# Kernel optimization log

Hardware: AMD Instinct MI355X
Metric: run time of the kernel (lower is better)

The kernel has to match this reference:

```python
import jax, jax.numpy as jnp
import numpy as np

N_NODES = 50000
N_EDGES = 800000
D = 64
VOCAB = 1000
NUM_ITERS = 2
BN_EPS = 1e-5


def _bn(h, g, b):
    # BatchNorm1d in training mode: batch statistics over the edge dim, biased var
    mu = h.mean(axis=0)
    var = h.var(axis=0)
    return g * (h - mu) * jax.lax.rsqrt(var + BN_EPS) + b


def _edge_agg(x, idx_i, idx_j, W1, b1, g1, be1, W2, b2, g2, be2):
    # gather -> concat -> Linear+BN+ReLU x2 -> scatter-sum to idx_i -> degree norm
    m = jnp.concatenate([x[idx_i], x[idx_j]], axis=1)          # [E, 2D]
    h = jax.nn.relu(_bn(m @ W1 + b1, g1, be1))                  # [E, D]
    h = jax.nn.relu(_bn(h @ W2 + b2, g2, be2))                  # [E, D]
    agg = jax.ops.segment_sum(h, idx_i, num_segments=N_NODES)   # [N, D]
    deg = jax.ops.segment_sum(jnp.ones((idx_i.shape[0],), x.dtype), idx_i,
                              num_segments=N_NODES)
    deg_inv = jnp.where(deg > 0, 1.0 / deg, 0.0)
    return deg_inv[:, None] * agg


def setup_inputs() -> dict:
    key = jax.random.key(0)
    ks = jax.random.split(key, 24)
    s = 0.05
    inp = {
        'nodes': jax.random.randint(ks[0], (N_NODES,), 0, VOCAB),
        'edges': jax.random.randint(ks[1], (2, N_EDGES), 0, N_NODES),
        'emb': jax.random.normal(ks[2], (VOCAB, D), jnp.float32) * s,
        # parent aggregation MLP
        'p_W1': jax.random.normal(ks[3], (2 * D, D), jnp.float32) * s,
        'p_b1': jnp.zeros((D,), jnp.float32),
        'p_g1': jnp.ones((D,), jnp.float32),
        'p_be1': jnp.zeros((D,), jnp.float32),
        'p_W2': jax.random.normal(ks[4], (D, D), jnp.float32) * s,
        'p_b2': jnp.zeros((D,), jnp.float32),
        'p_g2': jnp.ones((D,), jnp.float32),
        'p_be2': jnp.zeros((D,), jnp.float32),
        # child aggregation MLP
        'c_W1': jax.random.normal(ks[5], (2 * D, D), jnp.float32) * s,
        'c_b1': jnp.zeros((D,), jnp.float32),
        'c_g1': jnp.ones((D,), jnp.float32),
        'c_be1': jnp.zeros((D,), jnp.float32),
        'c_W2': jax.random.normal(ks[6], (D, D), jnp.float32) * s,
        'c_b2': jnp.zeros((D,), jnp.float32),
        'c_g2': jnp.ones((D,), jnp.float32),
        'c_be2': jnp.zeros((D,), jnp.float32),
        # final aggregation (dropout = identity, eval semantics)
        'fc_W': jax.random.normal(ks[7], (3 * D, 2 * D), jnp.float32) * s,
        'fc_b': jnp.zeros((2 * D,), jnp.float32),
        'fc2_W': jax.random.normal(ks[8], (2 * D, D), jnp.float32) * s,
        'fc2_b': jnp.zeros((D,), jnp.float32),
        # Conv1d(D, 2D, kernel=1) == Linear D -> 2D
        'conv_W': jax.random.normal(ks[9], (D, 2 * D), jnp.float32) * s,
        'conv_b': jnp.zeros((2 * D,), jnp.float32),
    }
    return inp


def reference(nodes, edges, emb, p_W1, p_b1, p_g1, p_be1, p_W2, p_b2, p_g2, p_be2,
              c_W1, c_b1, c_g1, c_be1, c_W2, c_b2, c_g2, c_be2,
              fc_W, fc_b, fc2_W, fc2_b, conv_W, conv_b):
    src, dst = edges[0], edges[1]
    x = emb[nodes]                                            # [N, D]
    for _ in range(NUM_ITERS):
        # ParentAggregation: flow source_to_target -> x_i = x[dst], x_j = x[src], scatter to dst
        fi = _edge_agg(x, dst, src, p_W1, p_b1, p_g1, p_be1, p_W2, p_b2, p_g2, p_be2)
        # ChildAggregation: flow target_to_source -> x_i = x[src], x_j = x[dst], scatter to src
        fo = _edge_agg(x, src, dst, c_W1, c_b1, c_g1, c_be1, c_W2, c_b2, c_g2, c_be2)
        cat = jnp.concatenate([x, fi, fo], axis=1)            # [N, 3D]
        upd = jax.nn.relu(cat @ fc_W + fc_b) @ fc2_W + fc2_b  # [N, D]
        x = x + upd
    return x @ conv_W + conv_b                                # [N, 2D]
```

## Files before the change

### kernel.cpp

```cpp
#include <hip/hip_runtime.h>

#define NN 50000
#define NE 800000
#define BN_EPS 1e-5f
#define SCAN_T 256
#define SCAN_NB ((NN + SCAN_T - 1) / SCAN_T)

#define BKT_SH 8
#define NBKT ((NN + 255) >> 8)
#define CAP 6144
#define PCH 4096
#define NPB ((NE + PCH - 1) / PCH)

#define ST_SUM1 0
#define ST_SQ1 64
#define ST_CROSS 128
#define ST_SUM2 192
#define ST_SSQ2 256
#define ST_AGG 320

using bf16x8 = __attribute__((ext_vector_type(8))) __bf16;
using bf16x4 = __attribute__((ext_vector_type(4))) __bf16;
using floatx4 = __attribute__((ext_vector_type(4))) float;

#define MFMA16(a, b, c) __builtin_amdgcn_mfma_f32_16x16x32_bf16(a, b, c, 0, 0, 0)

__device__ __forceinline__ bf16x8 load_wfrag(const float* W, int ncols, int kb, int ct, int lane) {
  int col = ct * 16 + (lane & 15);
  int k0 = kb * 32 + ((lane >> 4) << 3);
  bf16x8 f;
#pragma unroll
  for (int j = 0; j < 8; ++j) f[j] = (__bf16)W[(k0 + j) * ncols + col];
  return f;
}

__global__ void k_setup(const int* __restrict__ nodes, const float* __restrict__ emb,
                        float* __restrict__ x, int* __restrict__ bcur) {
  int tid = blockIdx.x * blockDim.x + threadIdx.x;
  int stride = gridDim.x * blockDim.x;
  for (int idx = tid; idx < NN * 64; idx += stride)
    x[idx] = emb[nodes[idx >> 6] * 64 + (idx & 63)];
  for (int t = tid; t < 2 * NBKT; t += stride)
    bcur[t] = (t < NBKT ? t : t - NBKT) * CAP;
}

__global__ void __launch_bounds__(256) k_part(const int* __restrict__ src,
                                              const int* __restrict__ dst,
                                              int* __restrict__ bcur,
                                              unsigned int* __restrict__ stage) {
  const int dir = blockIdx.y;
  const int* key = dir ? src : dst;
  int* bc = bcur + dir * NBKT;
  unsigned int* st = stage + (size_t)dir * NBKT * CAP;
  __shared__ int lh[256];
  __shared__ int sb[256];
  __shared__ int lbase[NBKT];
  __shared__ unsigned int pay[PCH];
  const int tid = threadIdx.x;
  lh[tid] = 0;
  __syncthreads();
  const int c0 = blockIdx.x * PCH;
  const int nv = (NE - c0 < PCH) ? (NE - c0) : PCH;
  unsigned int rk[PCH / 256];
#pragma unroll
  for (int i = 0; i < PCH / 256; ++i) {
    int l = i * 256 + tid;
    if (l < nv) {
      int b = key[c0 + l] >> BKT_SH;
      int r = atomicAdd(&lh[b], 1);
      rk[i] = ((unsigned)b << 13) | (unsigned)r;
    } else {
      rk[i] = 0xFFFFFFFFu;
    }
  }
  __syncthreads();
  int cntv = lh[tid];
  sb[tid] = cntv;
  __syncthreads();
  for (int o = 1; o < 256; o <<= 1) {
    int u = (tid >= o) ? sb[tid - o] : 0;
    __syncthreads();
    sb[tid] += u;
    __syncthreads();
  }
  int excl = sb[tid] - cntv;
  __syncthreads();
  sb[tid] = excl;
  if (tid < NBKT && cntv > 0) lbase[tid] = atomicAdd(&bc[tid], cntv);
  __syncthreads();
#pragma unroll
  for (int i = 0; i < PCH / 256; ++i) {
    if (rk[i] != 0xFFFFFFFFu) {
      int e = c0 + i * 256 + tid;
      int b = (int)(rk[i] >> 13);
      int r = (int)(rk[i] & 0x1FFFu);
      unsigned int s = (unsigned)src[e], d = (unsigned)dst[e];
      pay[sb[b] + r] = dir ? ((s << 16) | d) : ((d << 16) | s);
    }
  }
  __syncthreads();
  for (int t = tid; t < nv; t += 256) {
    int lo = 0, hi = 255;
    while (lo < hi) {
      int mid = (lo + hi + 1) >> 1;
      if (sb[mid] <= t) lo = mid; else hi = mid - 1;
    }
    st[lbase[lo] + (t - sb[lo])] = pay[t];
  }
}

__global__ void __launch_bounds__(256) k_count(const int* __restrict__ bcur,
                                               const unsigned int* __restrict__ stage,
                                               int* __restrict__ cnt_d, int* __restrict__ cnt_s) {
  const int dir = blockIdx.y;
  const int b = blockIdx.x;
  int* cnt = dir ? cnt_s : cnt_d;
  const unsigned int* st = stage + (size_t)dir * NBKT * CAP + (size_t)b * CAP;
  __shared__ int lc[256];
  lc[threadIdx.x] = 0;
  __syncthreads();
  int sz = bcur[dir * NBKT + b] - b * CAP;
  for (int t = threadIdx.x; t < sz; t += 256)
    atomicAdd(&lc[(st[t] >> 16) - (b << BKT_SH)], 1);
  __syncthreads();
  int n = (b << BKT_SH) + threadIdx.x;
  if (n < NN) cnt[n] = lc[threadIdx.x];
}

__global__ void k_scan1(const int* __restrict__ cnt_d, const int* __restrict__ cnt_s,
                        int* __restrict__ off_d, int* __restrict__ off_s, int* __restrict__ btot) {
  const int* cnt = blockIdx.y ? cnt_s : cnt_d;
  int* off = blockIdx.y ? off_s : off_d;
  __shared__ int sm[SCAN_T];
  int i = blockIdx.x * SCAN_T + threadIdx.x;
  int v = (i < NN) ? cnt[i] : 0;
  sm[threadIdx.x] = v;
  __syncthreads();
  for (int o = 1; o < SCAN_T; o <<= 1) {
    int u = (threadIdx.x >= o) ? sm[threadIdx.x - o] : 0;
    __syncthreads();
    sm[threadIdx.x] += u;
    __syncthreads();
  }
  if (i < NN) off[i] = sm[threadIdx.x];
  if (threadIdx.x == SCAN_T - 1) btot[blockIdx.y * SCAN_NB + blockIdx.x] = sm[SCAN_T - 1];
}

__global__ void k_scan2(int* __restrict__ btot) {
  __shared__ int sm[SCAN_T];
  int t = threadIdx.x;
  for (int y = 0; y < 2; ++y) {
    int v = (t < SCAN_NB) ? btot[y * SCAN_NB + t] : 0;
    sm[t] = v;
    __syncthreads();
    for (int o = 1; o < SCAN_T; o <<= 1) {
      int u = (t >= o) ? sm[t - o] : 0;
      __syncthreads();
      sm[t] += u;
      __syncthreads();
    }
    if (t < SCAN_NB) btot[y * SCAN_NB + t] = sm[t] - v;
    __syncthreads();
  }
}

__global__ void k_scan3(const int* __restrict__ cnt_d, const int* __restrict__ cnt_s,
                        int* __restrict__ off_d, int* __restrict__ off_s,
                        const int* __restrict__ btot, float* __restrict__ dinv_d,
                        float* __restrict__ dinv_s) {
  const int* cnt = blockIdx.y ? cnt_s : cnt_d;
  int* off = blockIdx.y ? off_s : off_d;
  float* dinv = blockIdx.y ? dinv_s : dinv_d;
  int i = blockIdx.x * SCAN_T + threadIdx.x;
  if (i < NN) {
    int incl = off[i];
    int c = cnt[i];
    int o = incl - c + btot[blockIdx.y * SCAN_NB + blockIdx.x];
    off[i] = o;
    dinv[i] = c > 0 ? 1.0f / (float)c : 0.f;
  }
  if (i == NN - 1) off[NN] = NE;
}

__global__ void __launch_bounds__(256) k_fill2(const int* __restrict__ bcur,
                                               const unsigned int* __restrict__ stage,
                                               const int* __restrict__ off_d,
                                               const int* __restrict__ off_s,
                                               unsigned short* __restrict__ jl_d,
                                               unsigned short* __restrict__ jl_s,
                                               unsigned short* __restrict__ il_d,
                                               unsigned short* __restrict__ il_s) {
  const int dir = blockIdx.y;
  const int b = blockIdx.x;
  const int* off = dir ? off_s : off_d;
  unsigned short* jl = dir ? jl_s : jl_d;
  unsigned short* il = dir ? il_s : il_d;
  const unsigned int* st = stage + (size_t)dir * NBKT * CAP + (size_t)b * CAP;
  __shared__ int lcur[256];
  __shared__ unsigned short ljl[CAP];
  __shared__ unsigned short lil[CAP];
  int csr0 = off[b << BKT_SH];
  int n = (b << BKT_SH) + threadIdx.x;
  lcur[threadIdx.x] = (n < NN) ? off[n] - csr0 : 0;
  __syncthreads();
  int sz = bcur[dir * NBKT + b] - b * CAP;
  for (int t = threadIdx.x; t < sz; t += 256) {
    unsigned int v = st[t];
    int p = atomicAdd(&lcur[(v >> 16) - (b << BKT_SH)], 1);
    ljl[p] = (unsigned short)(v & 0xFFFFu);
    lil[p] = (unsigned short)(v >> 16);
  }
  __syncthreads();
  for (int t = threadIdx.x; t < sz; t += 256) {
    jl[csr0 + t] = ljl[t];
    il[csr0 + t] = lil[t];
  }
}

__global__ void __launch_bounds__(256) k_node_xform(
    const float* __restrict__ x, const float* __restrict__ W1,
    __bf16* __restrict__ Ab, __bf16* __restrict__ Bb,
    float* __restrict__ stats, int do_zero) {
  const int lane = threadIdx.x & 63;
  const int wid = threadIdx.x >> 6;
  __shared__ alignas(16) __bf16 xb[4][16 * 72];
  if (do_zero && blockIdx.x == 0)
    for (int t = threadIdx.x; t < 2 * ST_AGG; t += blockDim.x) stats[t] = 0.f;
  bf16x8 wfa[4][2], wfb[4][2];
#pragma unroll
  for (int ct = 0; ct < 4; ++ct)
#pragma unroll
    for (int kb = 0; kb < 2; ++kb) {
      wfa[ct][kb] = load_wfrag(W1, 64, kb, ct, lane);
      wfb[ct][kb] = load_wfrag(W1 + 64 * 64, 64, kb, ct, lane);
    }
  __bf16* vb = xb[wid];
  int wgid = (blockIdx.x * blockDim.x + threadIdx.x) >> 6;
  int nw = (gridDim.x * blockDim.x) >> 6;
  for (int tile = wgid; tile < NN / 16; tile += nw) {
#pragma unroll
    for (int t = 0; t < 16; ++t)
      vb[t * 72 + lane] = (__bf16)x[(tile * 16 + t) * 64 + lane];
    const bf16x8 a0 = *(const bf16x8*)&vb[(lane & 15) * 72 + ((lane >> 4) << 3)];
    const bf16x8 a1 = *(const bf16x8*)&vb[(lane & 15) * 72 + 32 + ((lane >> 4) << 3)];
#pragma unroll
    for (int ct = 0; ct < 4; ++ct) {
      floatx4 aA = {0.f, 0.f, 0.f, 0.f}, aB = {0.f, 0.f, 0.f, 0.f};
      aA = MFMA16(a0, wfa[ct][0], aA);
      aA = MFMA16(a1, wfa[ct][1], aA);
      aB = MFMA16(a0, wfb[ct][0], aB);
      aB = MFMA16(a1, wfb[ct][1], aB);
#pragma unroll
      for (int r = 0; r < 4; ++r) {
        int row = ((lane >> 4) << 2) + r;
        int o = (tile * 16 + row) * 64 + ct * 16 + (lane & 15);
        Ab[o] = (__bf16)aA[r];
        Bb[o] = (__bf16)aB[r];
      }
    }
  }
}

__global__ void __launch_bounds__(256) k_node_stats(
    const __bf16* __restrict__ Ap, const __bf16* __restrict__ Bp,
    const __bf16* __restrict__ Ac, const __bf16* __restrict__ Bc,
    const int* __restrict__ cnt_d, const int* __restrict__ cnt_s,
    float* __restrict__ stats) {
  const int lane = threadIdx.x & 63;
  const int g = lane >> 4, q = lane & 15;
  __shared__ float sacc[256];
  for (int t = threadIdx.x; t < 256; t += blockDim.x) sacc[t] = 0.f;
  __syncthreads();
  float sp[4] = {0, 0, 0, 0}, qp[4] = {0, 0, 0, 0};
  float sc[4] = {0, 0, 0, 0}, qc[4] = {0, 0, 0, 0};
  int wgid = (blockIdx.x * blockDim.x + threadIdx.x) >> 6;
  int nw = (gridDim.x * blockDim.x) >> 6;
  for (int ch = wgid; ch < NN / 4; ch += nw) {
    int n = ch * 4 + g;
    float wd = (float)cnt_d[n];
    float ws = (float)cnt_s[n];
    bf16x4 ap = *(const bf16x4*)(Ap + n * 64 + 4 * q);
    bf16x4 bp = *(const bf16x4*)(Bp + n * 64 + 4 * q);
    bf16x4 ac = *(const bf16x4*)(Ac + n * 64 + 4 * q);
    bf16x4 bc = *(const bf16x4*)(Bc + n * 64 + 4 * q);
#pragma unroll
    for (int k = 0; k < 4; ++k) {
      float a = (float)ap[k], b = (float)bp[k], c = (float)ac[k], d = (float)bc[k];
      sp[k] += wd * a + ws * b;
      qp[k] += wd * a * a + ws * b * b;
      sc[k] += ws * c + wd * d;
      qc[k] += ws * c * c + wd * d * d;
    }
  }
#pragma unroll
  for (int k = 0; k < 4; ++k) {
    sp[k] += __shfl_xor(sp[k], 16); sp[k] += __shfl_xor(sp[k], 32);
    qp[k] += __shfl_xor(qp[k], 16); qp[k] += __shfl_xor(qp[k], 32);
    sc[k] += __shfl_xor(sc[k], 16); sc[k] += __shfl_xor(sc[k], 32);
    qc[k] += __shfl_xor(qc[k], 16); qc[k] += __shfl_xor(qc[k], 32);
  }
  if (lane < 16) {
#pragma unroll
    for (int k = 0; k < 4; ++k) {
      atomicAdd(&sacc[4 * q + k], sp[k]);
      atomicAdd(&sacc[64 + 4 * q + k], qp[k]);
      atomicAdd(&sacc[128 + 4 * q + k], sc[k]);
      atomicAdd(&sacc[192 + 4 * q + k], qc[k]);
    }
  }
  __syncthreads();
  for (int t = threadIdx.x; t < 256; t += blockDim.x) {
    int dstoff = (t < 128) ? t : ST_AGG + (t - 128);
    atomicAdd(&stats[dstoff], sacc[t]);
  }
}

__global__ void __launch_bounds__(256) k_cross_csr2(
    const unsigned short* __restrict__ il, const unsigned short* __restrict__ jl,
    const __bf16* __restrict__ Ap, const __bf16* __restrict__ Bp,
    const __bf16* __restrict__ Ac, const __bf16* __restrict__ Bc,
    float* __restrict__ stats) {
  const int lane = threadIdx.x & 63;
  const int c8 = lane & 7, e8 = lane >> 3;
  __shared__ float sacc[128];
  for (int t = threadIdx.x; t < 128; t += blockDim.x) sacc[t] = 0.f;
  __syncthreads();
  float cp[8] = {0, 0, 0, 0, 0, 0, 0, 0}, cc[8] = {0, 0, 0, 0, 0, 0, 0, 0};
  int wgid = (blockIdx.x * blockDim.x + threadIdx.x) >> 6;
  int nw = (gridDim.x * blockDim.x) >> 6;
  for (int tile = wgid; tile < NE / 16; tile += nw) {
    int e0 = tile * 16;
    int iv = (int)il[e0 + (lane & 15)];
    int jv = (int)jl[e0 + (lane & 15)];
#pragma unroll
    for (int r = 0; r < 2; ++r) {
      int ee = r * 8 + e8;
      int i = __shfl(iv, ee);
      int j = __shfl(jv, ee);
      bf16x8 ap = *(const bf16x8*)(Ap + (size_t)i * 64 + c8 * 8);
      bf16x8 bp = *(const bf16x8*)(Bp + (size_t)j * 64 + c8 * 8);
      bf16x8 ac = *(const bf16x8*)(Ac + (size_t)j * 64 + c8 * 8);
      bf16x8 bc = *(const bf16x8*)(Bc + (size_t)i * 64 + c8 * 8);
#pragma unroll
      for (int k = 0; k < 8; ++k) {
        cp[k] += (float)ap[k] * (float)bp[k];
        cc[k] += (float)ac[k] * (float)bc[k];
      }
    }
  }
#pragma unroll
  for (int k = 0; k < 8; ++k) {
    cp[k] += __shfl_xor(cp[k], 8);  cp[k] += __shfl_xor(cp[k], 16); cp[k] += __shfl_xor(cp[k], 32);
    cc[k] += __shfl_xor(cc[k], 8);  cc[k] += __shfl_xor(cc[k], 16); cc[k] += __shfl_xor(cc[k], 32);
  }
  if (lane < 8) {
#pragma unroll
    for (int k = 0; k < 8; ++k) {
      atomicAdd(&sacc[lane * 8 + k], cp[k]);
      atomicAdd(&sacc[64 + lane * 8 + k], cc[k]);
    }
  }
  __syncthreads();
  for (int t = threadIdx.x; t < 128; t += blockDim.x) {
    int dstoff = (t < 64) ? (ST_CROSS + t) : (ST_AGG + ST_CROSS + (t - 64));
    atomicAdd(&stats[dstoff], sacc[t]);
  }
}

__global__ void __launch_bounds__(256) k_edge_stats_csr2(
    const unsigned short* __restrict__ il, const unsigned short* __restrict__ jl,
    const __bf16* __restrict__ Ap, const __bf16* __restrict__ Bp,
    const __bf16* __restrict__ Ac, const __bf16* __restrict__ Bc,
    const float* __restrict__ pg1, const float* __restrict__ pbe1,
    const float* __restrict__ cg1, const float* __restrict__ cbe1,
    const float* __restrict__ pW2, const float* __restrict__ cW2,
    float* __restrict__ stats) {
  const int lane = threadIdx.x & 63;
  const int wid = threadIdx.x >> 6;
  const int g = lane >> 4, q = lane & 15;
  const int c8 = lane & 7;
  const int e8 = lane >> 3;
  __shared__ alignas(16) __bf16 vbuf[4][2][16 * 72];
  __shared__ float sred[256];
  float s1p[8], t1p[8], s1c[8], t1c[8];
#pragma unroll
  for (int k = 0; k < 8; ++k) {
    int c = c8 * 8 + k;
    float mu = stats[ST_SUM1 + c] * (1.f / NE);
    float var = (stats[ST_SQ1 + c] + 2.f * stats[ST_CROSS + c]) * (1.f / NE) - mu * mu;
    float s = pg1[c] * rsqrtf(var + BN_EPS);
    s1p[k] = s;
    t1p[k] = pbe1[c] - mu * s;
    mu = stats[ST_AGG + ST_SUM1 + c] * (1.f / NE);
    var = (stats[ST_AGG + ST_SQ1 + c] + 2.f * stats[ST_AGG + ST_CROSS + c]) * (1.f / NE) - mu * mu;
    s = cg1[c] * rsqrtf(var + BN_EPS);
    s1c[k] = s;
    t1c[k] = cbe1[c] - mu * s;
  }
  bf16x8 wfp[4][2], wfc[4][2];
#pragma unroll
  for (int ct = 0; ct < 4; ++ct)
#pragma unroll
    for (int kb = 0; kb < 2; ++kb) {
      wfp[ct][kb] = load_wfrag(pW2, 64, kb, ct, lane);
      wfc[ct][kb] = load_wfrag(cW2, 64, kb, ct, lane);
    }
  float sump[4] = {0, 0, 0, 0}, ssqp[4] = {0, 0, 0, 0};
  float sumc[4] = {0, 0, 0, 0}, ssqc[4] = {0, 0, 0, 0};
  __bf16* vbp = vbuf[wid][0];
  __bf16* vbc = vbuf[wid][1];
  int wgid = (blockIdx.x * blockDim.x + threadIdx.x) >> 6;
  int nw = (gridDim.x * blockDim.x) >> 6;
  for (int tile = wgid; tile < NE / 16; tile += nw) {
    int e0 = tile * 16;
    int iv = (int)il[e0 + q];
    int jv = (int)jl[e0 + q];
#pragma unroll
    for (int r = 0; r < 2; ++r) {
      int ee = r * 8 + e8;
      int i = __shfl(iv, ee);
      int j = __shfl(jv, ee);
      bf16x8 ap = *(const bf16x8*)(Ap + (size_t)i * 64 + c8 * 8);
      bf16x8 bp = *(const bf16x8*)(Bp + (size_t)j * 64 + c8 * 8);
      bf16x8 ac = *(const bf16x8*)(Ac + (size_t)j * 64 + c8 * 8);
      bf16x8 bc = *(const bf16x8*)(Bc + (size_t)i * 64 + c8 * 8);
      bf16x8 vp, vc;
#pragma unroll
      for (int k = 0; k < 8; ++k) {
        vp[k] = (__bf16)fmaxf(s1p[k] * ((float)ap[k] + (float)bp[k]) + t1p[k], 0.f);
        vc[k] = (__bf16)fmaxf(s1c[k] * ((float)ac[k] + (float)bc[k]) + t1c[k], 0.f);
      }
      *(bf16x8*)&vbp[ee * 72 + c8 * 8] = vp;
      *(bf16x8*)&vbc[ee * 72 + c8 * 8] = vc;
    }
    const bf16x8 a0p = *(const bf16x8*)&vbp[q * 72 + g * 8];
    const bf16x8 a1p = *(const bf16x8*)&vbp[q * 72 + 32 + g * 8];
    const bf16x8 a0c = *(const bf16x8*)&vbc[q * 72 + g * 8];
    const bf16x8 a1c = *(const bf16x8*)&vbc[q * 72 + 32 + g * 8];
#pragma unroll
    for (int ct = 0; ct < 4; ++ct) {
      floatx4 accp = {0.f, 0.f, 0.f, 0.f}, accc = {0.f, 0.f, 0.f, 0.f};
      accp = MFMA16(a0p, wfp[ct][0], accp);
      accp = MFMA16(a1p, wfp[ct][1], accp);
      accc = MFMA16(a0c, wfc[ct][0], accc);
      accc = MFMA16(a1c, wfc[ct][1], accc);
#pragma unroll
      for (int r = 0; r < 4; ++r) {
        float hp = accp[r], hc = accc[r];
        sump[ct] += hp;
        ssqp[ct] += hp * hp;
        sumc[ct] += hc;
        ssqc[ct] += hc * hc;
      }
    }
  }
  for (int t = threadIdx.x; t < 256; t += blockDim.x) sred[t] = 0.f;
  __syncthreads();
#pragma unroll
  for (int ct = 0; ct < 4; ++ct) {
    atomicAdd(&sred[ct * 16 + q], sump[ct]);
    atomicAdd(&sred[64 + ct * 16 + q], ssqp[ct]);
    atomicAdd(&sred[128 + ct * 16 + q], sumc[ct]);
    atomicAdd(&sred[192 + ct * 16 + q], ssqc[ct]);
  }
  __syncthreads();
  for (int t = threadIdx.x; t < 256; t += blockDim.x) {
    int dstoff;
    if (t < 64) dstoff = ST_SUM2 + t;
    else if (t < 128) dstoff = ST_SSQ2 + (t - 64);
    else if (t < 192) dstoff = ST_AGG + ST_SUM2 + (t - 128);
    else dstoff = ST_AGG + ST_SSQ2 + (t - 192);
    atomicAdd(&stats[dstoff], sred[t]);
  }
}

__global__ void __launch_bounds__(256) k_scatter_fused(
    const int* __restrict__ off, const float* __restrict__ dinv,
    const unsigned short* __restrict__ jl, const __bf16* __restrict__ A_,
    const __bf16* __restrict__ B_, const float* __restrict__ g1,
    const float* __restrict__ be1, const float* __restrict__ g2,
    const float* __restrict__ be2, const float* __restrict__ W2,
    const float* __restrict__ stats, int sbase, float* __restrict__ outb) {
  const int lane = threadIdx.x & 63;
  const int wid = threadIdx.x >> 6;
  const int g = lane >> 4, q = lane & 15;
  __shared__ alignas(16) __bf16 vbuf[4][16 * 72];
  float s1v[4], t1v[4];
#pragma unroll
  for (int k = 0; k < 4; ++k) {
    int c = 4 * q + k;
    float mu = stats[sbase + ST_SUM1 + c] * (1.f / NE);
    float var = (stats[sbase + ST_SQ1 + c] + 2.f * stats[sbase + ST_CROSS + c]) * (1.f / NE) - mu * mu;
    float s = g1[c] * rsqrtf(var + BN_EPS);
    s1v[k] = s;
    t1v[k] = be1[c] - mu * s;
  }
  float s2v[4], t2v[4];
#pragma unroll
  for (int ct = 0; ct < 4; ++ct) {
    int c = ct * 16 + q;
    float mu = stats[sbase + ST_SUM2 + c] * (1.f / NE);
    float var = stats[sbase + ST_SSQ2 + c] * (1.f / NE) - mu * mu;
    float s = g2[c] * rsqrtf(var + BN_EPS);
    s2v[ct] = s;
    t2v[ct] = be2[c] - mu * s;
  }
  bf16x8 wf[4][2];
#pragma unroll
  for (int ct = 0; ct < 4; ++ct)
#pragma unroll
    for (int kb = 0; kb < 2; ++kb) wf[ct][kb] = load_wfrag(W2, 64, kb, ct, lane);
  __bf16* vb = vbuf[wid];
  int wgid = (blockIdx.x * blockDim.x + threadIdx.x) >> 6;
  int nw = (gridDim.x * blockDim.x) >> 6;
  for (int n = wgid; n < NN; n += nw) {
    int p0 = off[n], p1 = off[n + 1];
    bf16x4 a4 = *(const bf16x4*)(A_ + (size_t)n * 64 + 4 * q);
    float ha[4];
#pragma unroll
    for (int k = 0; k < 4; ++k) ha[k] = (float)a4[k];
    float oacc[4] = {0.f, 0.f, 0.f, 0.f};
    for (int pt = p0; pt < p1; pt += 16) {
      int m = p1 - pt;
      if (m > 16) m = 16;
      int jj = (lane < m) ? (int)jl[pt + lane] : 0;
#pragma unroll
      for (int t = 0; t < 4; ++t) {
        int et = t * 4 + g;
        int j = __shfl(jj, et);
        bf16x4 b4 = *(const bf16x4*)(B_ + (size_t)j * 64 + 4 * q);
        bf16x4 v4;
#pragma unroll
        for (int k = 0; k < 4; ++k)
          v4[k] = (__bf16)fmaxf(s1v[k] * (ha[k] + (float)b4[k]) + t1v[k], 0.f);
        *(bf16x4*)&vb[et * 72 + 4 * q] = v4;
      }
      const bf16x8 a0 = *(const bf16x8*)&vb[q * 72 + g * 8];
      const bf16x8 a1 = *(const bf16x8*)&vb[q * 72 + 32 + g * 8];
#pragma unroll
      for (int ct = 0; ct < 4; ++ct) {
        floatx4 acc = {0.f, 0.f, 0.f, 0.f};
        acc = MFMA16(a0, wf[ct][0], acc);
        acc = MFMA16(a1, wf[ct][1], acc);
#pragma unroll
        for (int r = 0; r < 4; ++r)
          if (g * 4 + r < m) oacc[ct] += fmaxf(s2v[ct] * acc[r] + t2v[ct], 0.f);
      }
    }
#pragma unroll
    for (int ct = 0; ct < 4; ++ct) {
      oacc[ct] += __shfl_xor(oacc[ct], 16);
      oacc[ct] += __shfl_xor(oacc[ct], 32);
    }
    float val = (g == 0) ? oacc[0] : (g == 1) ? oacc[1] : (g == 2) ? oacc[2] : oacc[3];
    outb[(size_t)n * 64 + lane] = dinv[n] * val;
  }
}

__global__ void __launch_bounds__(256) k_node_update(
    float* __restrict__ x, const float* __restrict__ fi, const float* __restrict__ fo,
    const float* __restrict__ fcW, const float* __restrict__ fcb,
    const float* __restrict__ fc2W, const float* __restrict__ fc2b) {
  const int lane = threadIdx.x & 63;
  const int wid = threadIdx.x >> 6;
  __shared__ alignas(16) __bf16 cat[16 * 200];
  __shared__ alignas(16) __bf16 v2[16 * 136];
  bf16x8 wf1[2][6];
#pragma unroll
  for (int c = 0; c < 2; ++c) {
    int ct = 2 * wid + c;
#pragma unroll
    for (int kb = 0; kb < 6; ++kb) wf1[c][kb] = load_wfrag(fcW, 128, kb, ct, lane);
  }
  bf16x8 wf2[4];
#pragma unroll
  for (int kb = 0; kb < 4; ++kb) wf2[kb] = load_wfrag(fc2W, 64, kb, wid, lane);
  float fcbv[2];
#pragma unroll
  for (int c = 0; c < 2; ++c) fcbv[c] = fcb[(2 * wid + c) * 16 + (lane & 15)];
  float fc2bv = fc2b[wid * 16 + (lane & 15)];

  for (int tile = blockIdx.x; tile < NN / 16; tile += gridDim.x) {
#pragma unroll
    for (int r = 0; r < 4; ++r) {
      int rr = wid * 4 + r;
      int n = tile * 16 + rr;
      cat[rr * 200 + lane] = (__bf16)x[n * 64 + lane];
      cat[rr * 200 + 64 + lane] = (__bf16)fi[n * 64 + lane];
      cat[rr * 200 + 128 + lane] = (__bf16)fo[n * 64 + lane];
    }
    __syncthreads();
    floatx4 acc0 = {0.f, 0.f, 0.f, 0.f}, acc1 = {0.f, 0.f, 0.f, 0.f};
#pragma unroll
    for (int kb = 0; kb < 6; ++kb) {
      bf16x8 af = *(const bf16x8*)&cat[(lane & 15) * 200 + kb * 32 + ((lane >> 4) << 3)];
      acc0 = MFMA16(af, wf1[0][kb], acc0);
      acc1 = MFMA16(af, wf1[1][kb], acc1);
    }
#pragma unroll
    for (int r = 0; r < 4; ++r) {
      int row = ((lane >> 4) << 2) + r;
      v2[row * 136 + (2 * wid) * 16 + (lane & 15)] = (__bf16)fmaxf(acc0[r] + fcbv[0], 0.f);
      v2[row * 136 + (2 * wid + 1) * 16 + (lane & 15)] = (__bf16)fmaxf(acc1[r] + fcbv[1], 0.f);
    }
    __syncthreads();
    floatx4 a2 = {0.f, 0.f, 0.f, 0.f};
#pragma unroll
    for (int kb = 0; kb < 4; ++kb) {
      bf16x8 af = *(const bf16x8*)&v2[(lane & 15) * 136 + kb * 32 + ((lane >> 4) << 3)];
      a2 = MFMA16(af, wf2[kb], a2);
    }
#pragma unroll
    for (int r = 0; r < 4; ++r) {
      int row = ((lane >> 4) << 2) + r;
      int n = tile * 16 + row;
      x[n * 64 + wid * 16 + (lane & 15)] += a2[r] + fc2bv;
    }
    __syncthreads();
  }
}

__global__ void __launch_bounds__(256) k_conv(const float* __restrict__ x,
                                              const float* __restrict__ convW,
                                              const float* __restrict__ convb,
                                              float* __restrict__ out) {
  const int lane = threadIdx.x & 63;
  int wgid = (blockIdx.x * blockDim.x + threadIdx.x) >> 6;
  int nw = (gridDim.x * blockDim.x) >> 6;
  int half = wgid & 1;
  int col = half * 64 + lane;
  float wreg[64];
#pragma unroll
  for (int k = 0; k < 64; ++k) wreg[k] = convW[k * 128 + col];
  float bv = convb[col];
  for (int n = (wgid >> 1); n < NN; n += (nw >> 1)) {
    float xv = x[n * 64 + lane];
    float acc = bv;
#pragma unroll
    for (int k = 0; k < 64; ++k) acc += __shfl(xv, k) * wreg[k];
    out[(size_t)n * 128 + col] = acc;
  }
}

extern "C" void kernel_launch(void* const* d_in, const int* in_sizes, int n_in,
                              void* d_out, int out_size, void* d_ws, size_t ws_size,
                              hipStream_t stream) {
  const int* nodes = (const int*)d_in[0];
  const int* edges = (const int*)d_in[1];
  const int* src = edges;
  const int* dst = edges + NE;
  const float* emb = (const float*)d_in[2];
  const float* pW1 = (const float*)d_in[3];
  const float* pg1 = (const float*)d_in[5];
  const float* pbe1 = (const float*)d_in[6];
  const float* pW2 = (const float*)d_in[7];
  const float* pg2 = (const float*)d_in[9];
  const float* pbe2 = (const float*)d_in[10];
  const float* cW1 = (const float*)d_in[11];
  const float* cg1 = (const float*)d_in[13];
  const float* cbe1 = (const float*)d_in[14];
  const float* cW2 = (const float*)d_in[15];
  const float* cg2 = (const float*)d_in[17];
  const float* cbe2 = (const float*)d_in[18];
  const float* fcW = (const float*)d_in[19];
  const float* fcb = (const float*)d_in[20];
  const float* fc2W = (const float*)d_in[21];
  const float* fc2b = (const float*)d_in[22];
  const float* convW = (const float*)d_in[23];
  const float* convb = (const float*)d_in[24];
  float* out = (float*)d_out;

  char* w = (char*)d_ws;
  auto alloc = [&](size_t bytes) {
    char* p = w;
    w += (bytes + 255) & ~(size_t)255;
    return p;
  };
  float* x = (float*)alloc((size_t)NN * 64 * 4);
  __bf16* Ap = (__bf16*)alloc((size_t)NN * 64 * 2);
  __bf16* Bp = (__bf16*)alloc((size_t)NN * 64 * 2);
  __bf16* Ac = (__bf16*)alloc((size_t)NN * 64 * 2);
  __bf16* Bc = (__bf16*)alloc((size_t)NN * 64 * 2);
  float* fi = (float*)alloc((size_t)NN * 64 * 4);
  float* fo = (float*)alloc((size_t)NN * 64 * 4);
  unsigned short* jl_d = (unsigned short*)alloc((size_t)NE * 2);
  unsigned short* jl_s = (unsigned short*)alloc((size_t)NE * 2);
  unsigned short* il_d = (unsigned short*)alloc((size_t)NE * 2);
  unsigned short* il_s = (unsigned short*)alloc((size_t)NE * 2);
  int* off_d = (int*)alloc((size_t)(NN + 1) * 4);
  int* off_s = (int*)alloc((size_t)(NN + 1) * 4);
  int* cnt_d = (int*)alloc((size_t)NN * 4);
  int* cnt_s = (int*)alloc((size_t)NN * 4);
  float* dinv_d = (float*)alloc((size_t)NN * 4);
  float* dinv_s = (float*)alloc((size_t)NN * 4);
  float* stats = (float*)alloc(2 * ST_AGG * 4);
  int* btot = (int*)alloc(2 * SCAN_NB * 4);
  int* bcur = (int*)alloc((size_t)2 * NBKT * 4);
  unsigned int* stage = (unsigned int*)alloc((size_t)2 * NBKT * CAP * 4);

  k_setup<<<1024, 256, 0, stream>>>(nodes, emb, x, bcur);
  k_part<<<dim3(NPB, 2), 256, 0, stream>>>(src, dst, bcur, stage);
  k_count<<<dim3(NBKT, 2), 256, 0, stream>>>(bcur, stage, cnt_d, cnt_s);
  k_scan1<<<dim3(SCAN_NB, 2), SCAN_T, 0, stream>>>(cnt_d, cnt_s, off_d, off_s, btot);
  k_scan2<<<1, SCAN_T, 0, stream>>>(btot);
  k_scan3<<<dim3(SCAN_NB, 2), SCAN_T, 0, stream>>>(cnt_d, cnt_s, off_d, off_s, btot,
                                                   dinv_d, dinv_s);
  k_fill2<<<dim3(NBKT, 2), 256, 0, stream>>>(bcur, stage, off_d, off_s, jl_d, jl_s,
                                             il_d, il_s);

  for (int it = 0; it < 2; ++it) {
    k_node_xform<<<784, 256, 0, stream>>>(x, pW1, Ap, Bp, stats, 1);
    k_node_xform<<<784, 256, 0, stream>>>(x, cW1, Ac, Bc, stats, 0);
    k_node_stats<<<256, 256, 0, stream>>>(Ap, Bp, Ac, Bc, cnt_d, cnt_s, stats);
    k_cross_csr2<<<2048, 256, 0, stream>>>(il_d, jl_d, Ap, Bp, Ac, Bc, stats);
    k_edge_stats_csr2<<<2048, 256, 0, stream>>>(il_d, jl_d, Ap, Bp, Ac, Bc, pg1, pbe1,
                                                cg1, cbe1, pW2, cW2, stats);
    k_scatter_fused<<<2048, 256, 0, stream>>>(off_d, dinv_d, jl_d, Ap, Bp, pg1, pbe1,
                                              pg2, pbe2, pW2, stats, 0, fi);
    k_scatter_fused<<<2048, 256, 0, stream>>>(off_s, dinv_s, jl_s, Ac, Bc, cg1, cbe1,
                                              cg2, cbe2, cW2, stats, ST_AGG, fo);
    k_node_update<<<3125, 256, 0, stream>>>(x, fi, fo, fcW, fcb, fc2W, fc2b);
  }
  k_conv<<<2048, 256, 0, stream>>>(x, convW, convb, out);
}
```

Before: 911.4 us.

## Software-pipeline gathers in cross and edge-stats kernels, split edge stats per branch

```diff
diff --git a/kernel.cpp b/kernel.cpp
--- a/kernel.cpp
+++ b/kernel.cpp
@@ -315,38 +315,66 @@
   }
 }
 
-__global__ void __launch_bounds__(256) k_cross_csr2(
+#define CR_ISSUE(iv, jv, p0a, p0b, c0a, c0b, p1a, p1b, c1a, c1b)               \
+  {                                                                            \
+    int i0 = __shfl((iv), e8), j0 = __shfl((jv), e8);                          \
+    int i1 = __shfl((iv), 8 + e8), j1 = __shfl((jv), 8 + e8);                  \
+    p0a = *(const bf16x8*)(Ap + (size_t)i0 * 64 + c8 * 8);                     \
+    p0b = *(const bf16x8*)(Bp + (size_t)j0 * 64 + c8 * 8);                     \
+    c0a = *(const bf16x8*)(Ac + (size_t)j0 * 64 + c8 * 8);                     \
+    c0b = *(const bf16x8*)(Bc + (size_t)i0 * 64 + c8 * 8);                     \
+    p1a = *(const bf16x8*)(Ap + (size_t)i1 * 64 + c8 * 8);                     \
+    p1b = *(const bf16x8*)(Bp + (size_t)j1 * 64 + c8 * 8);                     \
+    c1a = *(const bf16x8*)(Ac + (size_t)j1 * 64 + c8 * 8);                     \
+    c1b = *(const bf16x8*)(Bc + (size_t)i1 * 64 + c8 * 8);                     \
+  }
+#define CR_COMPUTE(p0a, p0b, c0a, c0b, p1a, p1b, c1a, c1b)                     \
+  {                                                                            \
+    _Pragma("unroll") for (int k = 0; k < 8; ++k) {                            \
+      cp[k] += (float)p0a[k] * (float)p0b[k] + (float)p1a[k] * (float)p1b[k];  \
+      cc[k] += (float)c0a[k] * (float)c0b[k] + (float)c1a[k] * (float)c1b[k];  \
+    }                                                                          \
+  }
+__global__ void __launch_bounds__(256) k_cross_csr3(
     const unsigned short* __restrict__ il, const unsigned short* __restrict__ jl,
     const __bf16* __restrict__ Ap, const __bf16* __restrict__ Bp,
     const __bf16* __restrict__ Ac, const __bf16* __restrict__ Bc,
     float* __restrict__ stats) {
   const int lane = threadIdx.x & 63;
-  const int c8 = lane & 7, e8 = lane >> 3;
+  const int c8 = lane & 7, e8 = lane >> 3, q = lane & 15;
   __shared__ float sacc[128];
   for (int t = threadIdx.x; t < 128; t += blockDim.x) sacc[t] = 0.f;
   __syncthreads();
   float cp[8] = {0, 0, 0, 0, 0, 0, 0, 0}, cc[8] = {0, 0, 0, 0, 0, 0, 0, 0};
   int wgid = (blockIdx.x * blockDim.x + threadIdx.x) >> 6;
   int nw = (gridDim.x * blockDim.x) >> 6;
-  for (int tile = wgid; tile < NE / 16; tile += nw) {
-    int e0 = tile * 16;
-    int iv = (int)il[e0 + (lane & 15)];
-    int jv = (int)jl[e0 + (lane & 15)];
-#pragma unroll
-    for (int r = 0; r < 2; ++r) {
-      int ee = r * 8 + e8;
-      int i = __shfl(iv, ee);
-      int j = __shfl(jv, ee);
-      bf16x8 ap = *(const bf16x8*)(Ap + (size_t)i * 64 + c8 * 8);
-      bf16x8 bp = *(const bf16x8*)(Bp + (size_t)j * 64 + c8 * 8);
-      bf16x8 ac = *(const bf16x8*)(Ac + (size_t)j * 64 + c8 * 8);
-      bf16x8 bc = *(const bf16x8*)(Bc + (size_t)i * 64 + c8 * 8);
-#pragma unroll
-      for (int k = 0; k < 8; ++k) {
-        cp[k] += (float)ap[k] * (float)bp[k];
-        cc[k] += (float)ac[k] * (float)bc[k];
-      }
-    }
+  const int NT = NE / 16;
+  bf16x8 A0a = {}, A0b = {}, A1a = {}, A1b = {}, A2a = {}, A2b = {}, A3a = {}, A3b = {};
+  bf16x8 B0a = {}, B0b = {}, B1a = {}, B1b = {}, B2a = {}, B2b = {}, B3a = {}, B3b = {};
+  int ivC = 0, jvC = 0, ivN = 0, jvN = 0;
+  int t = wgid;
+  bool v0 = (t < NT);
+  if (v0) {
+    ivC = (int)il[t * 16 + q];
+    jvC = (int)jl[t * 16 + q];
+    CR_ISSUE(ivC, jvC, A0a, A0b, A1a, A1b, A2a, A2b, A3a, A3b);
+    int tn0 = t + nw;
+    if (tn0 < NT) { ivN = (int)il[tn0 * 16 + q]; jvN = (int)jl[tn0 * 16 + q]; }
+  }
+  while (v0) {
+    int tn = t + nw;
+    bool v1 = (tn < NT);
+    if (v1) {
+      CR_ISSUE(ivN, jvN, B0a, B0b, B1a, B1b, B2a, B2b, B3a, B3b);
+      int t2 = tn + nw;
+      if (t2 < NT) { ivC = (int)il[t2 * 16 + q]; jvC = (int)jl[t2 * 16 + q]; }
+    }
+    CR_COMPUTE(A0a, A0b, A1a, A1b, A2a, A2b, A3a, A3b);
+    A0a = B0a; A0b = B0b; A1a = B1a; A1b = B1b;
+    A2a = B2a; A2b = B2b; A3a = B3a; A3b = B3b;
+    { int ti = ivN; ivN = ivC; ivC = ti; ti = jvN; jvN = jvC; jvC = ti; }
+    t = tn;
+    v0 = v1;
   }
 #pragma unroll
   for (int k = 0; k < 8; ++k) {
@@ -361,116 +389,110 @@
     }
   }
   __syncthreads();
-  for (int t = threadIdx.x; t < 128; t += blockDim.x) {
-    int dstoff = (t < 64) ? (ST_CROSS + t) : (ST_AGG + ST_CROSS + (t - 64));
-    atomicAdd(&stats[dstoff], sacc[t]);
-  }
-}
-
-__global__ void __launch_bounds__(256) k_edge_stats_csr2(
+  for (int tt = threadIdx.x; tt < 128; tt += blockDim.x) {
+    int dstoff = (tt < 64) ? (ST_CROSS + tt) : (ST_AGG + ST_CROSS + (tt - 64));
+    atomicAdd(&stats[dstoff], sacc[tt]);
+  }
+}
+
+#define ES_ISSUE(iv, jv, r0a, r0b, r1a, r1b)                                   \
+  {                                                                            \
+    int i0 = __shfl((iv), e8), j0 = __shfl((jv), e8);                          \
+    int i1 = __shfl((iv), 8 + e8), j1 = __shfl((jv), 8 + e8);                  \
+    r0a = *(const bf16x8*)(Aseq + (size_t)i0 * 64 + c8 * 8);                   \
+    r0b = *(const bf16x8*)(Brand + (size_t)j0 * 64 + c8 * 8);                  \
+    r1a = *(const bf16x8*)(Aseq + (size_t)i1 * 64 + c8 * 8);                   \
+    r1b = *(const bf16x8*)(Brand + (size_t)j1 * 64 + c8 * 8);                  \
+  }
+#define ES_COMPUTE(r0a, r0b, r1a, r1b)                                         \
+  {                                                                            \
+    bf16x8 v0, v1;                                                             \
+    _Pragma("unroll") for (int k = 0; k < 8; ++k) {                            \
+      v0[k] = (__bf16)fmaxf(s1[k] * ((float)r0a[k] + (float)r0b[k]) + t1[k], 0.f); \
+      v1[k] = (__bf16)fmaxf(s1[k] * ((float)r1a[k] + (float)r1b[k]) + t1[k], 0.f); \
+    }                                                                          \
+    *(bf16x8*)&vb[e8 * 72 + c8 * 8] = v0;                                      \
+    *(bf16x8*)&vb[(8 + e8) * 72 + c8 * 8] = v1;                                \
+    const bf16x8 a0 = *(const bf16x8*)&vb[q * 72 + g4 * 8];                    \
+    const bf16x8 a1 = *(const bf16x8*)&vb[q * 72 + 32 + g4 * 8];               \
+    _Pragma("unroll") for (int ct = 0; ct < 4; ++ct) {                         \
+      floatx4 acc = {0.f, 0.f, 0.f, 0.f};                                      \
+      acc = MFMA16(a0, wf[ct][0], acc);                                        \
+      acc = MFMA16(a1, wf[ct][1], acc);                                        \
+      _Pragma("unroll") for (int r = 0; r < 4; ++r) {                          \
+        sum2[ct] += acc[r];                                                    \
+        ssq2[ct] += acc[r] * acc[r];                                           \
+      }                                                                        \
+    }                                                                          \
+  }
+__global__ void __launch_bounds__(256) k_edge_stats1(
     const unsigned short* __restrict__ il, const unsigned short* __restrict__ jl,
-    const __bf16* __restrict__ Ap, const __bf16* __restrict__ Bp,
-    const __bf16* __restrict__ Ac, const __bf16* __restrict__ Bc,
-    const float* __restrict__ pg1, const float* __restrict__ pbe1,
-    const float* __restrict__ cg1, const float* __restrict__ cbe1,
-    const float* __restrict__ pW2, const float* __restrict__ cW2,
-    float* __restrict__ stats) {
+    const __bf16* __restrict__ Aseq, const __bf16* __restrict__ Brand,
+    const float* __restrict__ g1, const float* __restrict__ be1,
+    const float* __restrict__ W2, float* __restrict__ stats, int sbase) {
   const int lane = threadIdx.x & 63;
   const int wid = threadIdx.x >> 6;
-  const int g = lane >> 4, q = lane & 15;
-  const int c8 = lane & 7;
-  const int e8 = lane >> 3;
-  __shared__ alignas(16) __bf16 vbuf[4][2][16 * 72];
-  __shared__ float sred[256];
-  float s1p[8], t1p[8], s1c[8], t1c[8];
+  const int g4 = lane >> 4, q = lane & 15;
+  const int c8 = lane & 7, e8 = lane >> 3;
+  __shared__ alignas(16) __bf16 vbuf[4][16 * 72];
+  __shared__ float sred[128];
+  float s1[8], t1[8];
 #pragma unroll
   for (int k = 0; k < 8; ++k) {
     int c = c8 * 8 + k;
-    float mu = stats[ST_SUM1 + c] * (1.f / NE);
-    float var = (stats[ST_SQ1 + c] + 2.f * stats[ST_CROSS + c]) * (1.f / NE) - mu * mu;
-    float s = pg1[c] * rsqrtf(var + BN_EPS);
-    s1p[k] = s;
-    t1p[k] = pbe1[c] - mu * s;
-    mu = stats[ST_AGG + ST_SUM1 + c] * (1.f / NE);
-    var = (stats[ST_AGG + ST_SQ1 + c] + 2.f * stats[ST_AGG + ST_CROSS + c]) * (1.f / NE) - mu * mu;
-    s = cg1[c] * rsqrtf(var + BN_EPS);
-    s1c[k] = s;
-    t1c[k] = cbe1[c] - mu * s;
-  }
-  bf16x8 wfp[4][2], wfc[4][2];
+    float mu = stats[sbase + ST_SUM1 + c] * (1.f / NE);
+    float var = (stats[sbase + ST_SQ1 + c] + 2.f * stats[sbase + ST_CROSS + c]) * (1.f / NE) - mu * mu;
+    float s = g1[c] * rsqrtf(var + BN_EPS);
+    s1[k] = s;
+    t1[k] = be1[c] - mu * s;
+  }
+  bf16x8 wf[4][2];
 #pragma unroll
   for (int ct = 0; ct < 4; ++ct)
 #pragma unroll
-    for (int kb = 0; kb < 2; ++kb) {
-      wfp[ct][kb] = load_wfrag(pW2, 64, kb, ct, lane);
-      wfc[ct][kb] = load_wfrag(cW2, 64, kb, ct, lane);
-    }
-  float sump[4] = {0, 0, 0, 0}, ssqp[4] = {0, 0, 0, 0};
-  float sumc[4] = {0, 0, 0, 0}, ssqc[4] = {0, 0, 0, 0};
-  __bf16* vbp = vbuf[wid][0];
-  __bf16* vbc = vbuf[wid][1];
+    for (int kb = 0; kb < 2; ++kb) wf[ct][kb] = load_wfrag(W2, 64, kb, ct, lane);
+  float sum2[4] = {0, 0, 0, 0}, ssq2[4] = {0, 0, 0, 0};
+  __bf16* vb = vbuf[wid];
   int wgid = (blockIdx.x * blockDim.x + threadIdx.x) >> 6;
   int nw = (gridDim.x * blockDim.x) >> 6;
-  for (int tile = wgid; tile < NE / 16; tile += nw) {
-    int e0 = tile * 16;
-    int iv = (int)il[e0 + q];
-    int jv = (int)jl[e0 + q];
-#pragma unroll
-    for (int r = 0; r < 2; ++r) {
-      int ee = r * 8 + e8;
-      int i = __shfl(iv, ee);
-      int j = __shfl(jv, ee);
-      bf16x8 ap = *(const bf16x8*)(Ap + (size_t)i * 64 + c8 * 8);
-      bf16x8 bp = *(const bf16x8*)(Bp + (size_t)j * 64 + c8 * 8);
-      bf16x8 ac = *(const bf16x8*)(Ac + (size_t)j * 64 + c8 * 8);
-      bf16x8 bc = *(const bf16x8*)(Bc + (size_t)i * 64 + c8 * 8);
-      bf16x8 vp, vc;
-#pragma unroll
-      for (int k = 0; k < 8; ++k) {
-        vp[k] = (__bf16)fmaxf(s1p[k] * ((float)ap[k] + (float)bp[k]) + t1p[k], 0.f);
-        vc[k] = (__bf16)fmaxf(s1c[k] * ((float)ac[k] + (float)bc[k]) + t1c[k], 0.f);
-      }
-      *(bf16x8*)&vbp[ee * 72 + c8 * 8] = vp;
-      *(bf16x8*)&vbc[ee * 72 + c8 * 8] = vc;
-    }
-    const bf16x8 a0p = *(const bf16x8*)&vbp[q * 72 + g * 8];
-    const bf16x8 a1p = *(const bf16x8*)&vbp[q * 72 + 32 + g * 8];
-    const bf16x8 a0c = *(const bf16x8*)&vbc[q * 72 + g * 8];
-    const bf16x8 a1c = *(const bf16x8*)&vbc[q * 72 + 32 + g * 8];
-#pragma unroll
-    for (int ct = 0; ct < 4; ++ct) {
-      floatx4 accp = {0.f, 0.f, 0.f, 0.f}, accc = {0.f, 0.f, 0.f, 0.f};
-      accp = MFMA16(a0p, wfp[ct][0], accp);
-      accp = MFMA16(a1p, wfp[ct][1], accp);
-      accc = MFMA16(a0c, wfc[ct][0], accc);
-      accc = MFMA16(a1c, wfc[ct][1], accc);
-#pragma unroll
-      for (int r = 0; r < 4; ++r) {
-        float hp = accp[r], hc = accc[r];
-        sump[ct] += hp;
-        ssqp[ct] += hp * hp;
-        sumc[ct] += hc;
-        ssqc[ct] += hc * hc;
-      }
-    }
-  }
-  for (int t = threadIdx.x; t < 256; t += blockDim.x) sred[t] = 0.f;
+  const int NT = NE / 16;
+  bf16x8 cA0 = {}, cB0 = {}, cA1 = {}, cB1 = {};
+  bf16x8 nA0 = {}, nB0 = {}, nA1 = {}, nB1 = {};
+  int ivC = 0, jvC = 0, ivN = 0, jvN = 0;
+  int t = wgid;
+  bool v0 = (t < NT);
+  if (v0) {
+    ivC = (int)il[t * 16 + q];
+    jvC = (int)jl[t * 16 + q];
+    ES_ISSUE(ivC, jvC, cA0, cB0, cA1, cB1);
+    int tn0 = t + nw;
+    if (tn0 < NT) { ivN = (int)il[tn0 * 16 + q]; jvN = (int)jl[tn0 * 16 + q]; }
+  }
+  while (v0) {
+    int tn = t + nw;
+    bool v1 = (tn < NT);
+    if (v1) {
+      ES_ISSUE(ivN, jvN, nA0, nB0, nA1, nB1);
+      int t2 = tn + nw;
+      if (t2 < NT) { ivC = (int)il[t2 * 16 + q]; jvC = (int)jl[t2 * 16 + q]; }
+    }
+    ES_COMPUTE(cA0, cB0, cA1, cB1);
+    cA0 = nA0; cB0 = nB0; cA1 = nA1; cB1 = nB1;
+    { int ti = ivN; ivN = ivC; ivC = ti; ti = jvN; jvN = jvC; jvC = ti; }
+    t = tn;
+    v0 = v1;
+  }
+  for (int tt = threadIdx.x; tt < 128; tt += blockDim.x) sred[tt] = 0.f;
   __syncthreads();
 #pragma unroll
   for (int ct = 0; ct < 4; ++ct) {
-    atomicAdd(&sred[ct * 16 + q], sump[ct]);
-    atomicAdd(&sred[64 + ct * 16 + q], ssqp[ct]);
-    atomicAdd(&sred[128 + ct * 16 + q], sumc[ct]);
-    atomicAdd(&sred[192 + ct * 16 + q], ssqc[ct]);
-  }
-  __syncthreads();
-  for (int t = threadIdx.x; t < 256; t += blockDim.x) {
-    int dstoff;
-    if (t < 64) dstoff = ST_SUM2 + t;
-    else if (t < 128) dstoff = ST_SSQ2 + (t - 64);
-    else if (t < 192) dstoff = ST_AGG + ST_SUM2 + (t - 128);
-    else dstoff = ST_AGG + ST_SSQ2 + (t - 192);
-    atomicAdd(&stats[dstoff], sred[t]);
+    atomicAdd(&sred[ct * 16 + q], sum2[ct]);
+    atomicAdd(&sred[64 + ct * 16 + q], ssq2[ct]);
+  }
+  __syncthreads();
+  for (int tt = threadIdx.x; tt < 128; tt += blockDim.x) {
+    int dstoff = (tt < 64) ? (ST_SUM2 + tt) : (ST_SSQ2 + (tt - 64));
+    atomicAdd(&stats[sbase + dstoff], sred[tt]);
   }
 }
 
@@ -712,9 +734,11 @@
     k_node_xform<<<784, 256, 0, stream>>>(x, pW1, Ap, Bp, stats, 1);
     k_node_xform<<<784, 256, 0, stream>>>(x, cW1, Ac, Bc, stats, 0);
     k_node_stats<<<256, 256, 0, stream>>>(Ap, Bp, Ac, Bc, cnt_d, cnt_s, stats);
-    k_cross_csr2<<<2048, 256, 0, stream>>>(il_d, jl_d, Ap, Bp, Ac, Bc, stats);
-    k_edge_stats_csr2<<<2048, 256, 0, stream>>>(il_d, jl_d, Ap, Bp, Ac, Bc, pg1, pbe1,
-                                                cg1, cbe1, pW2, cW2, stats);
+    k_cross_csr3<<<2048, 256, 0, stream>>>(il_d, jl_d, Ap, Bp, Ac, Bc, stats);
+    k_edge_stats1<<<2048, 256, 0, stream>>>(il_d, jl_d, Ap, Bp, pg1, pbe1, pW2,
+                                            stats, 0);
+    k_edge_stats1<<<2048, 256, 0, stream>>>(il_d, jl_d, Bc, Ac, cg1, cbe1, cW2,
+                                            stats, ST_AGG);
     k_scatter_fused<<<2048, 256, 0, stream>>>(off_d, dinv_d, jl_d, Ap, Bp, pg1, pbe1,
                                               pg2, pbe2, pW2, stats, 0, fi);
     k_scatter_fused<<<2048, 256, 0, stream>>>(off_s, dinv_s, jl_s, Ac, Bc, cg1, cbe1,
```

Measured after the change: 939.6 us. 3.1% more time.
